# Kernel tuning notes

Hardware: AMD Instinct MI355X
Metric: run time of the kernel (lower is better)

## Reference

```python
import jax, jax.numpy as jnp
import numpy as np
import math

C = 512
H = W = 64
B = 4
NUM_GROUPS = 32
EPS = 1e-6
NUM_HEADS = 1  # num_head_channels=None -> 1 head


def group_norm(x, scale, bias):
    # x: [B, H, W, C] -> normalize per group of channels over (H, W, group-chans)
    b, h, w, c = x.shape
    xg = x.reshape(b, h, w, NUM_GROUPS, c // NUM_GROUPS)
    mean = xg.mean(axis=(1, 2, 4), keepdims=True)
    var = xg.var(axis=(1, 2, 4), keepdims=True)
    xg = (xg - mean) * jax.lax.rsqrt(var + EPS)
    x = xg.reshape(b, h, w, c)
    return x * scale + bias


def setup_inputs() -> dict:
    key = jax.random.key(0)
    ks = jax.random.split(key, 5)
    s = 1.0 / math.sqrt(C)
    return {
        "hidden_states": jax.random.normal(ks[0], (B, H, W, C), jnp.float32),
        "gn_scale": jnp.ones((C,), jnp.float32),
        "gn_bias": jnp.zeros((C,), jnp.float32),
        "Wq": jax.random.normal(ks[1], (C, C), jnp.float32) * s,
        "bq": jnp.zeros((C,), jnp.float32),
        "Wk": jax.random.normal(ks[2], (C, C), jnp.float32) * s,
        "bk": jnp.zeros((C,), jnp.float32),
        "Wv": jax.random.normal(ks[3], (C, C), jnp.float32) * s,
        "bv": jnp.zeros((C,), jnp.float32),
        "Wp": jax.random.normal(ks[4], (C, C), jnp.float32) * s,
        "bp": jnp.zeros((C,), jnp.float32),
    }


def reference(hidden_states, gn_scale, gn_bias, Wq, bq, Wk, bk, Wv, bv, Wp, bp):
    residual = hidden_states
    b, h, w, c = hidden_states.shape
    x = group_norm(hidden_states, gn_scale, gn_bias)
    x = x.reshape(b, h * w, c)  # [B, N, C]

    hd = c // NUM_HEADS
    def heads(t):  # [B, N, C] -> [B, nh, N, hd]
        return t.reshape(b, h * w, NUM_HEADS, hd).transpose(0, 2, 1, 3)

    q = heads(x @ Wq + bq)
    k = heads(x @ Wk + bk)
    v = heads(x @ Wv + bv)

    scale = 1.0 / math.sqrt(math.sqrt(c / NUM_HEADS))
    attn = jnp.einsum('bhqc,bhkc->bhqk', q * scale, k * scale)
    attn = jax.nn.softmax(attn, axis=-1)
    out = jnp.einsum('bhkc,bhqk->bhqc', v, attn)  # [B, nh, N, hd]
    out = out.transpose(0, 2, 1, 3).reshape(b, h * w, c)
    out = out @ Wp + bp
    out = out.reshape(b, h, w, c)
    return out + residual
```

## Files before the change

### kernel.cpp

```cpp
#include <hip/hip_runtime.h>
#include <hip/hip_bf16.h>

typedef __attribute__((ext_vector_type(8))) short bf16x8;
typedef __attribute__((ext_vector_type(4))) float f32x4;
typedef __attribute__((ext_vector_type(4))) unsigned short u16x4;

#define MFMA16(a, b, c) __builtin_amdgcn_mfma_f32_16x16x32_bf16(a, b, c, 0, 0, 0)

#define SCALE 0.21022410381342865f

__device__ __forceinline__ unsigned short f2bf(float f) {
    union { float f; unsigned u; } v; v.f = f;
    unsigned r = v.u + 0x7FFF + ((v.u >> 16) & 1);
    return (unsigned short)(r >> 16);
}

__device__ __forceinline__ unsigned cvtpk(float lo, float hi) {
    unsigned r;
    asm("v_cvt_pk_bf16_f32 %0, %1, %2" : "=v"(r) : "v"(lo), "v"(hi));
    return r;
}

typedef __attribute__((address_space(3))) void lds_void;
typedef const __attribute__((address_space(1))) void gbl_void;
__device__ __forceinline__ void g2l16(const void* g, void* l) {
    __builtin_amdgcn_global_load_lds((gbl_void*)g, (lds_void*)l, 16, 0, 0);
}

#define PHASE_BARRIER() do { \
    asm volatile("s_waitcnt vmcnt(0) lgkmcnt(0)" ::: "memory"); \
    __builtin_amdgcn_s_barrier(); \
    __builtin_amdgcn_sched_barrier(0); \
} while (0)

#define LGKM_BARRIER() do { \
    asm volatile("s_waitcnt lgkmcnt(0)" ::: "memory"); \
    __builtin_amdgcn_s_barrier(); \
    __builtin_amdgcn_sched_barrier(0); \
} while (0)

__global__ __launch_bounds__(256) void gn_stats(
    const float* __restrict__ x, float2* __restrict__ gstats)
{
    int id = blockIdx.x;
    int b = id >> 8, rem = id & 255;
    int g = rem >> 3, sl = rem & 7;
    int t = threadIdx.x;
    const float4* xf4 = (const float4*)x;
    size_t base4 = (size_t)b * (4096 * 128) + g * 4;

    float s = 0.f, ss = 0.f;
#pragma unroll
    for (int i = 0; i < 8; ++i) {
        int flat = i * 256 + t;
        int hw = sl * 512 + (flat >> 2), c4 = flat & 3;
        float4 v = xf4[base4 + (size_t)hw * 128 + c4];
        s  += v.x + v.y + v.z + v.w;
        ss += v.x * v.x + v.y * v.y + v.z * v.z + v.w * v.w;
    }
    for (int m = 32; m >= 1; m >>= 1) { s += __shfl_xor(s, m); ss += __shfl_xor(ss, m); }
    __shared__ float rs_[4], rss_[4];
    int wv = t >> 6;
    if ((t & 63) == 0) { rs_[wv] = s; rss_[wv] = ss; }
    __syncthreads();
    if (t == 0) {
        float2 o;
        o.x = rs_[0] + rs_[1] + rs_[2] + rs_[3];
        o.y = rss_[0] + rss_[1] + rss_[2] + rss_[3];
        gstats[id] = o;
    }
}

__global__ __launch_bounds__(256) void gn_apply(
    const float* __restrict__ x, const float* __restrict__ gamma,
    const float* __restrict__ beta, const float2* __restrict__ gstats,
    unsigned short* __restrict__ xn)
{
    int id = blockIdx.x;
    int b = id >> 9, rem = id & 511;
    int g = rem >> 4, sl = rem & 15;
    int t = threadIdx.x;

    float s = 0.f, ss = 0.f;
#pragma unroll
    for (int i = 0; i < 8; ++i) {
        float2 p = gstats[(b * 32 + g) * 8 + i];
        s += p.x; ss += p.y;
    }
    float mean = s * (1.f / 65536.f);
    float var  = ss * (1.f / 65536.f) - mean * mean;
    float rstd = rsqrtf(var + 1e-6f);

    const float4* xf4 = (const float4*)x;
    const float4* g4 = (const float4*)gamma;
    const float4* b4 = (const float4*)beta;
    size_t base4 = (size_t)b * (4096 * 128) + g * 4;
#pragma unroll
    for (int i = 0; i < 4; ++i) {
        int flat = i * 256 + t;
        int hw = sl * 256 + (flat >> 2), c4 = flat & 3;
        float4 v  = xf4[base4 + (size_t)hw * 128 + c4];
        float4 gm = g4[g * 4 + c4], bt = b4[g * 4 + c4];
        u16x4 o;
        o.x = f2bf((v.x - mean) * rstd * gm.x + bt.x);
        o.y = f2bf((v.y - mean) * rstd * gm.y + bt.y);
        o.z = f2bf((v.z - mean) * rstd * gm.z + bt.z);
        o.w = f2bf((v.w - mean) * rstd * gm.w + bt.w);
        *(u16x4*)&xn[(size_t)(b * 4096 + hw) * 512 + g * 16 + c4 * 4] = o;
    }
}

__global__ __launch_bounds__(256) void wprep(
    const float* __restrict__ Wq, const float* __restrict__ Wk,
    const float* __restrict__ Wv, const float* __restrict__ Wp,
    unsigned short* __restrict__ wqkvt, unsigned short* __restrict__ wpt)
{
    int idx = blockIdx.x * 256 + threadIdx.x;
    if (idx < 786432) {
        int n = idx >> 9, k = idx & 511;
        int j = n >> 9, nn = n & 511;
        const float* W = (j == 0) ? Wq : (j == 1) ? Wk : Wv;
        wqkvt[idx] = f2bf(W[k * 512 + nn]);
    } else {
        int i2 = idx - 786432;
        int n = i2 >> 9, k = i2 & 511;
        wpt[i2] = f2bf(Wp[k * 512 + n]);
    }
}

template <int MODE>
__global__ __launch_bounds__(256, 3) void gemm_kernel(
    const unsigned short* __restrict__ A, const unsigned short* __restrict__ Bt,
    const float* __restrict__ bias_q, const float* __restrict__ bias_k,
    const float* __restrict__ bias_v, const float* __restrict__ bias_p,
    const float* __restrict__ resid,
    unsigned short* __restrict__ Cbf, float* __restrict__ Cf)
{
    int m0 = blockIdx.x * 128;
    int n0 = blockIdx.y * 128;
    int t = threadIdx.x;
    int l = t & 63, w = t >> 6;
    int wm = w >> 1, wn = w & 1;
    int lr = l & 15, lg = l >> 4;

    __shared__ __align__(16) unsigned short lds[16384];
    unsigned short* As = lds;
    unsigned short* Bs = lds + 8192;

    const unsigned short* A_ = A + (size_t)m0 * 512;
    const unsigned short* B_ = Bt + (size_t)n0 * 512;

    auto stage = [&](int s) {
        int k0 = s * 64;
#pragma unroll
        for (int c = 0; c < 4; ++c) {
            int flat = c * 256 + t;
            int row = flat >> 3, u = flat & 7;
            g2l16(A_ + (size_t)row * 512 + k0 + ((u ^ (row & 7)) << 3),
                  As + (flat << 3));
        }
#pragma unroll
        for (int c = 0; c < 4; ++c) {
            int flat = c * 256 + t;
            int row = flat >> 3, u = flat & 7;
            g2l16(B_ + (size_t)row * 512 + k0 + ((u ^ (row & 7)) << 3),
                  Bs + (flat << 3));
        }
    };

    f32x4 acc[4][4];
#pragma unroll
    for (int i = 0; i < 4; ++i)
#pragma unroll
        for (int j = 0; j < 4; ++j) acc[i][j] = f32x4{0.f, 0.f, 0.f, 0.f};

    for (int s = 0; s < 8; ++s) {
        if (s) LGKM_BARRIER();
        stage(s);
        PHASE_BARRIER();
        __builtin_amdgcn_s_setprio(1);
#pragma unroll
        for (int ks = 0; ks < 2; ++ks) {
            bf16x8 af[4], bfr[4];
#pragma unroll
            for (int mi = 0; mi < 4; ++mi) {
                int row = wm * 64 + mi * 16 + lr;
                af[mi] = *(const bf16x8*)&As[(row * 8 + ((ks * 4 + lg) ^ (row & 7))) << 3];
            }
#pragma unroll
            for (int ni = 0; ni < 4; ++ni) {
                int row = wn * 64 + ni * 16 + lr;
                bfr[ni] = *(const bf16x8*)&Bs[(row * 8 + ((ks * 4 + lg) ^ (row & 7))) << 3];
            }
#pragma unroll
            for (int mi = 0; mi < 4; ++mi)
#pragma unroll
                for (int ni = 0; ni < 4; ++ni)
                    acc[mi][ni] = MFMA16(af[mi], bfr[ni], acc[mi][ni]);
        }
        __builtin_amdgcn_s_setprio(0);
    }

#pragma unroll
    for (int mi = 0; mi < 4; ++mi)
#pragma unroll
        for (int ni = 0; ni < 4; ++ni)
#pragma unroll
            for (int r = 0; r < 4; ++r) {
                int row = m0 + wm * 64 + mi * 16 + lg * 4 + r;
                int col = n0 + wn * 64 + ni * 16 + lr;
                float val = acc[mi][ni][r];
                if (MODE == 0) {
                    float bias, scl;
                    if (col < 512)       { bias = bias_q[col];        scl = SCALE; }
                    else if (col < 1024) { bias = bias_k[col - 512];  scl = SCALE; }
                    else                 { bias = bias_v[col - 1024]; scl = 1.0f;  }
                    Cbf[(size_t)row * 1536 + col] = f2bf((val + bias) * scl);
                } else {
                    Cf[(size_t)row * 512 + col] =
                        val + bias_p[col] + resid[(size_t)row * 512 + col];
                }
            }
}

__global__ __launch_bounds__(256) void vtrans(
    const unsigned short* __restrict__ qkv, unsigned short* __restrict__ vT)
{
    int n0 = blockIdx.x * 64, d0 = blockIdx.y * 64, b = blockIdx.z;
    int t = threadIdx.x;
    __shared__ unsigned short tile[64][72];
    for (int c = 0; c < 2; ++c) {
        int flat = c * 256 + t;
        int r = flat >> 3, cc = (flat & 7) * 8;
        *(bf16x8*)&tile[r][cc] =
            *(const bf16x8*)&qkv[(size_t)(b * 4096 + n0 + r) * 1536 + 1024 + d0 + cc];
    }
    __syncthreads();
    for (int c = 0; c < 2; ++c) {
        int flat = c * 256 + t;
        int dr = flat >> 3, nc = (flat & 7) * 8;
        bf16x8 v;
        for (int j = 0; j < 8; ++j) v[j] = (short)tile[nc + j][dr];
        *(bf16x8*)&vT[((size_t)b * 512 + d0 + dr) * 4096 + n0 + nc] = v;
    }
}

__global__ __launch_bounds__(256, 3) void qk_kernel(
    const unsigned short* __restrict__ qkv, unsigned short* __restrict__ P,
    float* __restrict__ lpart, int b0)
{
    int W = blockIdx.x;
    int xcd = W & 7, i = W >> 3;
    int bb = xcd >> 2;
    int nb = (xcd & 3) * 8 + (i & 7);
    int mb = i >> 3;
    int m0 = mb * 128, n0 = nb * 128;
    int b = b0 + bb;

    int t = threadIdx.x, l = t & 63, w = t >> 6;
    int wm = w >> 1, wn = w & 1;
    int lr = l & 15, lg = l >> 4;

    __shared__ __align__(16) unsigned short lds[16896];
    unsigned short* As = lds;
    unsigned short* Bs = lds + 8192;
    float* Lw = (float*)(lds + 16384);

    const unsigned short* A_ = qkv + (size_t)(b * 4096 + m0) * 1536 + 512;
    const unsigned short* B_ = qkv + (size_t)(b * 4096 + n0) * 1536;

    auto stage = [&](int s) {
        int k0 = s * 64;
#pragma unroll
        for (int c = 0; c < 4; ++c) {
            int flat = c * 256 + t;
            int row = flat >> 3, u = flat & 7;
            g2l16(A_ + (size_t)row * 1536 + k0 + ((u ^ (row & 7)) << 3),
                  As + (flat << 3));
        }
#pragma unroll
        for (int c = 0; c < 4; ++c) {
            int flat = c * 256 + t;
            int row = flat >> 3, u = flat & 7;
            g2l16(B_ + (size_t)row * 1536 + k0 + ((u ^ (row & 7)) << 3),
                  Bs + (flat << 3));
        }
    };

    f32x4 acc[4][4];
#pragma unroll
    for (int mi = 0; mi < 4; ++mi)
#pragma unroll
        for (int ni = 0; ni < 4; ++ni) acc[mi][ni] = f32x4{0.f, 0.f, 0.f, 0.f};

    for (int s = 0; s < 8; ++s) {
        if (s) LGKM_BARRIER();
        stage(s);
        PHASE_BARRIER();
        __builtin_amdgcn_s_setprio(1);
#pragma unroll
        for (int ks = 0; ks < 2; ++ks) {
            bf16x8 af[4], bfr[4];
#pragma unroll
            for (int mi = 0; mi < 4; ++mi) {
                int row = wm * 64 + mi * 16 + lr;
                af[mi] = *(const bf16x8*)&As[(row * 8 + ((ks * 4 + lg) ^ (row & 7))) << 3];
            }
#pragma unroll
            for (int ni = 0; ni < 4; ++ni) {
                int row = wn * 64 + ni * 16 + lr;
                bfr[ni] = *(const bf16x8*)&Bs[(row * 8 + ((ks * 4 + lg) ^ (row & 7))) << 3];
            }
#pragma unroll
            for (int mi = 0; mi < 4; ++mi)
#pragma unroll
                for (int ni = 0; ni < 4; ++ni)
                    acc[mi][ni] = MFMA16(af[mi], bfr[ni], acc[mi][ni]);
        }
        __builtin_amdgcn_s_setprio(0);
    }
    LGKM_BARRIER();

    unsigned short* Pl = lds;
    {
        float sums[4] = {0.f, 0.f, 0.f, 0.f};
#pragma unroll
        for (int mi = 0; mi < 4; ++mi) {
            int u = wm * 8 + mi * 2 + (lg >> 1);
            int half = lg & 1;
#pragma unroll
            for (int ni = 0; ni < 4; ++ni) {
                float p0 = __expf(acc[mi][ni][0]);
                float p1 = __expf(acc[mi][ni][1]);
                float p2 = __expf(acc[mi][ni][2]);
                float p3 = __expf(acc[mi][ni][3]);
                sums[ni] += p0 + p1 + p2 + p3;
                int q = wn * 64 + ni * 16 + lr;
                unsigned* dst = (unsigned*)&((char*)Pl)[
                    q * 256 + ((u ^ (q & 7)) << 4) + (half << 3)];
                dst[0] = cvtpk(p0, p1);
                dst[1] = cvtpk(p2, p3);
            }
        }
#pragma unroll
        for (int ni = 0; ni < 4; ++ni) {
            float v = sums[ni];
            v += __shfl_xor(v, 16);
            v += __shfl_xor(v, 32);
            if (lg == 0) Lw[wm * 128 + wn * 64 + ni * 16 + lr] = v;
        }
    }
    LGKM_BARRIER();

    if (t < 128)
        lpart[(size_t)(bb * 32 + mb) * 4096 + n0 + t] = Lw[t] + Lw[128 + t];

#pragma unroll
    for (int c = 0; c < 8; ++c) {
        int flat = c * 256 + t;
        int row = flat >> 4, u = flat & 15;
        *(bf16x8*)&P[((size_t)(bb * 4096 + n0 + row)) * 4096 + m0 + u * 8] =
            *(const bf16x8*)&((char*)Pl)[row * 256 + ((u ^ (row & 7)) << 4)];
    }
}

__global__ __launch_bounds__(256) void lred_kernel(
    const float* __restrict__ lpart, float* __restrict__ lsum)
{
    int rr = blockIdx.x * 256 + threadIdx.x;
    int bb = rr >> 12, r = rr & 4095;
    float s = 0.f;
#pragma unroll
    for (int sl = 0; sl < 32; ++sl)
        s += lpart[(size_t)(bb * 32 + sl) * 4096 + r];
    lsum[rr] = 1.0f / s;
}

__global__ __launch_bounds__(512) void pv_kernel(
    const unsigned short* __restrict__ P, const unsigned short* __restrict__ vT,
    const float* __restrict__ linv, unsigned short* __restrict__ outb, int b0)
{
    int m0 = blockIdx.x * 128, n0 = blockIdx.y * 128, bb = blockIdx.z;
    int b = b0 + bb;
    int t = threadIdx.x, l = t & 63, w = t >> 6;
    int wm = w >> 2, wn = w & 3;
    int lr = l & 15, lg = l >> 4;

    __shared__ __align__(16) unsigned short lds[49152];
    unsigned short* As = lds;
    unsigned short* Bs = lds + 24576;

    const unsigned short* A_ = P + (size_t)(bb * 4096 + m0) * 4096;
    const unsigned short* B_ = vT + ((size_t)b * 512 + n0) * 4096;

    auto stage = [&](int s, int buf) {
        int k0 = s * 64;
        unsigned short* ad = As + buf * 8192;
        unsigned short* bd = Bs + buf * 8192;
#pragma unroll
        for (int c = 0; c < 2; ++c) {
            int flat = c * 512 + t;
            int row = flat >> 3, u = flat & 7;
            g2l16(A_ + (size_t)row * 4096 + k0 + ((u ^ (row & 7)) << 3),
                  ad + (flat << 3));
        }
#pragma unroll
        for (int c = 0; c < 2; ++c) {
            int flat = c * 512 + t;
            int row = flat >> 3, u = flat & 7;
            g2l16(B_ + (size_t)row * 4096 + k0 + ((u ^ (row & 7)) << 3),
                  bd + (flat << 3));
        }
    };

    f32x4 acc[4][2];
#pragma unroll
    for (int i = 0; i < 4; ++i)
#pragma unroll
        for (int j = 0; j < 2; ++j) acc[i][j] = f32x4{0.f, 0.f, 0.f, 0.f};

    stage(0, 0);
    stage(1, 1);
    asm volatile("s_waitcnt vmcnt(4)" ::: "memory");
    __builtin_amdgcn_s_barrier();
    __builtin_amdgcn_sched_barrier(0);

    for (int s = 0; s < 64; ++s) {
        if (s + 2 < 64) stage(s + 2, (s + 2) % 3);
        const unsigned short* Al = As + (s % 3) * 8192;
        const unsigned short* Bl = Bs + (s % 3) * 8192;
        __builtin_amdgcn_s_setprio(1);
#pragma unroll
        for (int ks = 0; ks < 2; ++ks) {
            bf16x8 af[4], bfr[2];
#pragma unroll
            for (int mi = 0; mi < 4; ++mi) {
                int row = wm * 64 + mi * 16 + lr;
                af[mi] = *(const bf16x8*)&Al[(row * 8 + ((ks * 4 + lg) ^ (row & 7))) << 3];
            }
#pragma unroll
            for (int ni = 0; ni < 2; ++ni) {
                int row = wn * 32 + ni * 16 + lr;
                bfr[ni] = *(const bf16x8*)&Bl[(row * 8 + ((ks * 4 + lg) ^ (row & 7))) << 3];
            }
#pragma unroll
            for (int mi = 0; mi < 4; ++mi)
#pragma unroll
                for (int ni = 0; ni < 2; ++ni)
                    acc[mi][ni] = MFMA16(af[mi], bfr[ni], acc[mi][ni]);
        }
        __builtin_amdgcn_s_setprio(0);
        if (s < 62) asm volatile("s_waitcnt vmcnt(4) lgkmcnt(0)" ::: "memory");
        else        asm volatile("s_waitcnt vmcnt(0) lgkmcnt(0)" ::: "memory");
        __builtin_amdgcn_s_barrier();
        __builtin_amdgcn_sched_barrier(0);
    }

#pragma unroll
    for (int mi = 0; mi < 4; ++mi)
#pragma unroll
        for (int r = 0; r < 4; ++r) {
            int row = m0 + wm * 64 + mi * 16 + lg * 4 + r;
            float inv = linv[bb * 4096 + row];
#pragma unroll
            for (int ni = 0; ni < 2; ++ni) {
                int col = n0 + wn * 32 + ni * 16 + lr;
                outb[(size_t)(b * 4096 + row) * 512 + col] =
                    f2bf(acc[mi][ni][r] * inv);
            }
        }
}

extern "C" void kernel_launch(void* const* d_in, const int* in_sizes, int n_in,
                              void* d_out, int out_size, void* d_ws, size_t ws_size,
                              hipStream_t stream)
{
    const float* x     = (const float*)d_in[0];
    const float* gamma = (const float*)d_in[1];
    const float* beta  = (const float*)d_in[2];
    const float* Wq = (const float*)d_in[3];
    const float* bq = (const float*)d_in[4];
    const float* Wk = (const float*)d_in[5];
    const float* bk = (const float*)d_in[6];
    const float* Wv = (const float*)d_in[7];
    const float* bv = (const float*)d_in[8];
    const float* Wp = (const float*)d_in[9];
    const float* bp = (const float*)d_in[10];
    float* out = (float*)d_out;

    unsigned short* xn    = (unsigned short*)d_ws;
    unsigned short* wqkvt = xn + (size_t)16384 * 512;
    unsigned short* wpt   = wqkvt + (size_t)1536 * 512;
    unsigned short* qkv   = wpt + (size_t)512 * 512;
    unsigned short* vT    = qkv + (size_t)16384 * 1536;
    unsigned short* P     = vT + (size_t)4 * 512 * 4096;
    float* lpart = (float*)(P + (size_t)2 * 4096 * 4096);
    float* linv  = lpart + (size_t)128 * 4096;
    float2* gstats = (float2*)(linv + 8192);

    gn_stats<<<dim3(1024), dim3(256), 0, stream>>>(x, gstats);
    gn_apply<<<dim3(2048), dim3(256), 0, stream>>>(x, gamma, beta, gstats, xn);
    wprep<<<dim3(4096), dim3(256), 0, stream>>>(Wq, Wk, Wv, Wp, wqkvt, wpt);
    gemm_kernel<0><<<dim3(128, 12), dim3(256), 0, stream>>>(
        xn, wqkvt, bq, bk, bv, nullptr, nullptr, qkv, nullptr);
    vtrans<<<dim3(64, 8, 4), dim3(256), 0, stream>>>(qkv, vT);

    for (int b0 = 0; b0 < 4; b0 += 2) {
        qk_kernel<<<dim3(2048), dim3(256), 0, stream>>>(qkv, P, lpart, b0);
        lred_kernel<<<dim3(32), dim3(256), 0, stream>>>(lpart, linv);
        pv_kernel<<<dim3(32, 4, 2), dim3(512), 0, stream>>>(P, vT, linv, xn, b0);
    }

    gemm_kernel<1><<<dim3(128, 4), dim3(256), 0, stream>>>(
        xn, wpt, nullptr, nullptr, nullptr, bp, x, nullptr, out);
}
```

Before: 252.8 us.

## Enlarge QK tiles to 256x256 with double-buffered, phase-interleaved async loads

The QK^T kernel moves from 128x128 tiles with 256 threads to 256x256 tiles with 512 threads (8 waves), so the grid shrinks from 2048 to 512 blocks. Global-to-LDS loads are double-buffered and issued per half-tile, interleaved across four compute phases, with explicit vmcnt waits replacing the per-stage load-then-compute barrier. The larger tile raises operand reuse per byte loaded and hides load latency. In exchange it uses about 130KB of LDS (one block per CU), more accumulator registers and fewer blocks. The lpart partial-sum count and the reduction kernel are adjusted to match.

```diff
diff --git a/kernel.cpp b/kernel.cpp
--- a/kernel.cpp
+++ b/kernel.cpp
@@ -245,122 +245,165 @@
     }
 }
 
-__global__ __launch_bounds__(256, 3) void qk_kernel(
+__global__ __launch_bounds__(512, 1) void qk_kernel(
     const unsigned short* __restrict__ qkv, unsigned short* __restrict__ P,
     float* __restrict__ lpart, int b0)
 {
     int W = blockIdx.x;
     int xcd = W & 7, i = W >> 3;
     int bb = xcd >> 2;
-    int nb = (xcd & 3) * 8 + (i & 7);
-    int mb = i >> 3;
-    int m0 = mb * 128, n0 = nb * 128;
+    int nb = (xcd & 3) * 4 + (i & 3);
+    int mb = i >> 2;
+    int m0 = mb * 256, n0 = nb * 256;
     int b = b0 + bb;
 
     int t = threadIdx.x, l = t & 63, w = t >> 6;
-    int wm = w >> 1, wn = w & 1;
+    int wm = w >> 2, wn = w & 3;
     int lr = l & 15, lg = l >> 4;
 
-    __shared__ __align__(16) unsigned short lds[16896];
-    unsigned short* As = lds;
-    unsigned short* Bs = lds + 8192;
-    float* Lw = (float*)(lds + 16384);
-
-    const unsigned short* A_ = qkv + (size_t)(b * 4096 + m0) * 1536 + 512;
-    const unsigned short* B_ = qkv + (size_t)(b * 4096 + n0) * 1536;
-
-    auto stage = [&](int s) {
+    __shared__ __align__(16) unsigned short lds[66560];
+    float* Lw = (float*)(lds + 65536);
+
+    const unsigned short* Ksrc = qkv + 512;
+    const unsigned short* Qsrc = qkv;
+
+    auto stageA = [&](int s, int h) {
         int k0 = s * 64;
-#pragma unroll
-        for (int c = 0; c < 4; ++c) {
-            int flat = c * 256 + t;
+        unsigned short* dst = lds + ((s & 1) * 2 + h) * 8192;
+#pragma unroll
+        for (int c = 0; c < 2; ++c) {
+            int flat = c * 512 + t;
             int row = flat >> 3, u = flat & 7;
-            g2l16(A_ + (size_t)row * 1536 + k0 + ((u ^ (row & 7)) << 3),
-                  As + (flat << 3));
-        }
-#pragma unroll
-        for (int c = 0; c < 4; ++c) {
-            int flat = c * 256 + t;
+            int kv = m0 + h * 128 + row;
+            g2l16(Ksrc + (size_t)(b * 4096 + kv) * 1536 + k0 + ((u ^ (row & 7)) << 3),
+                  dst + (flat << 3));
+        }
+    };
+    auto stageB = [&](int s, int h) {
+        int k0 = s * 64;
+        unsigned short* dst = lds + 32768 + ((s & 1) * 2 + h) * 8192;
+#pragma unroll
+        for (int c = 0; c < 2; ++c) {
+            int flat = c * 512 + t;
             int row = flat >> 3, u = flat & 7;
-            g2l16(B_ + (size_t)row * 1536 + k0 + ((u ^ (row & 7)) << 3),
-                  Bs + (flat << 3));
+            int q = n0 + h * 128 + row;
+            g2l16(Qsrc + (size_t)(b * 4096 + q) * 1536 + k0 + ((u ^ (row & 7)) << 3),
+                  dst + (flat << 3));
         }
     };
 
-    f32x4 acc[4][4];
-#pragma unroll
-    for (int mi = 0; mi < 4; ++mi)
+    f32x4 acc[8][4];
+#pragma unroll
+    for (int mi = 0; mi < 8; ++mi)
 #pragma unroll
         for (int ni = 0; ni < 4; ++ni) acc[mi][ni] = f32x4{0.f, 0.f, 0.f, 0.f};
 
+    stageA(0, 0); stageA(0, 1); stageB(0, 0); stageB(0, 1);
+    stageA(1, 0); stageB(1, 0);
+    asm volatile("s_waitcnt vmcnt(4)" ::: "memory");
+    __builtin_amdgcn_s_barrier();
+    __builtin_amdgcn_sched_barrier(0);
+
     for (int s = 0; s < 8; ++s) {
-        if (s) LGKM_BARRIER();
-        stage(s);
-        PHASE_BARRIER();
-        __builtin_amdgcn_s_setprio(1);
-#pragma unroll
-        for (int ks = 0; ks < 2; ++ks) {
-            bf16x8 af[4], bfr[4];
+#pragma unroll
+        for (int ph = 0; ph < 4; ++ph) {
+            const int mh = ph & 1, nh = ph >> 1;
+            const unsigned short* Abase = lds + ((s & 1) * 2 + mh) * 8192;
+            const unsigned short* Bbase = lds + 32768 + ((s & 1) * 2 + nh) * 8192;
+            bf16x8 af[4][2], bfr[2][2];
 #pragma unroll
             for (int mi = 0; mi < 4; ++mi) {
                 int row = wm * 64 + mi * 16 + lr;
-                af[mi] = *(const bf16x8*)&As[(row * 8 + ((ks * 4 + lg) ^ (row & 7))) << 3];
-            }
-#pragma unroll
-            for (int ni = 0; ni < 4; ++ni) {
-                int row = wn * 64 + ni * 16 + lr;
-                bfr[ni] = *(const bf16x8*)&Bs[(row * 8 + ((ks * 4 + lg) ^ (row & 7))) << 3];
-            }
+#pragma unroll
+                for (int ks = 0; ks < 2; ++ks)
+                    af[mi][ks] = *(const bf16x8*)&Abase[
+                        (row * 8 + ((ks * 4 + lg) ^ (row & 7))) << 3];
+            }
+#pragma unroll
+            for (int ni = 0; ni < 2; ++ni) {
+                int row = wn * 32 + ni * 16 + lr;
+#pragma unroll
+                for (int ks = 0; ks < 2; ++ks)
+                    bfr[ni][ks] = *(const bf16x8*)&Bbase[
+                        (row * 8 + ((ks * 4 + lg) ^ (row & 7))) << 3];
+            }
+            if (ph == 0) { if (s + 1 < 8) stageA(s + 1, 1); }
+            if (ph == 1) { if (s + 1 < 8) stageB(s + 1, 1); }
+            if (ph == 2) { if (s + 2 < 8) stageB(s + 2, 0); }
+            if (ph == 3) { if (s + 2 < 8) stageA(s + 2, 0); }
+
+            __builtin_amdgcn_s_barrier();
+            asm volatile("s_waitcnt lgkmcnt(0)" ::: "memory");
+            __builtin_amdgcn_sched_barrier(0);
+
+            __builtin_amdgcn_s_setprio(1);
 #pragma unroll
             for (int mi = 0; mi < 4; ++mi)
 #pragma unroll
-                for (int ni = 0; ni < 4; ++ni)
-                    acc[mi][ni] = MFMA16(af[mi], bfr[ni], acc[mi][ni]);
-        }
-        __builtin_amdgcn_s_setprio(0);
-    }
-    LGKM_BARRIER();
+                for (int ni = 0; ni < 2; ++ni)
+#pragma unroll
+                    for (int ks = 0; ks < 2; ++ks)
+                        acc[mh * 4 + mi][nh * 2 + ni] =
+                            MFMA16(af[mi][ks], bfr[ni][ks], acc[mh * 4 + mi][nh * 2 + ni]);
+            __builtin_amdgcn_s_setprio(0);
+
+            if (s < 6 || (s == 6 && ph < 2))
+                asm volatile("s_waitcnt vmcnt(8)" ::: "memory");
+            else
+                asm volatile("s_waitcnt vmcnt(0)" ::: "memory");
+            __builtin_amdgcn_s_barrier();
+            __builtin_amdgcn_sched_barrier(0);
+        }
+    }
 
     unsigned short* Pl = lds;
     {
         float sums[4] = {0.f, 0.f, 0.f, 0.f};
 #pragma unroll
-        for (int mi = 0; mi < 4; ++mi) {
-            int u = wm * 8 + mi * 2 + (lg >> 1);
-            int half = lg & 1;
-#pragma unroll
-            for (int ni = 0; ni < 4; ++ni) {
-                float p0 = __expf(acc[mi][ni][0]);
-                float p1 = __expf(acc[mi][ni][1]);
-                float p2 = __expf(acc[mi][ni][2]);
-                float p3 = __expf(acc[mi][ni][3]);
-                sums[ni] += p0 + p1 + p2 + p3;
-                int q = wn * 64 + ni * 16 + lr;
-                unsigned* dst = (unsigned*)&((char*)Pl)[
-                    q * 256 + ((u ^ (q & 7)) << 4) + (half << 3)];
-                dst[0] = cvtpk(p0, p1);
-                dst[1] = cvtpk(p2, p3);
-            }
-        }
-#pragma unroll
-        for (int ni = 0; ni < 4; ++ni) {
-            float v = sums[ni];
-            v += __shfl_xor(v, 16);
-            v += __shfl_xor(v, 32);
-            if (lg == 0) Lw[wm * 128 + wn * 64 + ni * 16 + lr] = v;
-        }
+        for (int mh = 0; mh < 2; ++mh)
+#pragma unroll
+            for (int mi = 0; mi < 4; ++mi) {
+                int u = mh * 16 + wm * 8 + mi * 2 + (lg >> 1);
+                int half = lg & 1;
+#pragma unroll
+                for (int nh = 0; nh < 2; ++nh)
+#pragma unroll
+                    for (int ni = 0; ni < 2; ++ni) {
+                        int j = nh * 2 + ni;
+                        float p0 = __expf(acc[mh * 4 + mi][j][0]);
+                        float p1 = __expf(acc[mh * 4 + mi][j][1]);
+                        float p2 = __expf(acc[mh * 4 + mi][j][2]);
+                        float p3 = __expf(acc[mh * 4 + mi][j][3]);
+                        sums[j] += p0 + p1 + p2 + p3;
+                        int qL = nh * 128 + wn * 32 + ni * 16 + lr;
+                        unsigned* dst = (unsigned*)&((char*)Pl)[
+                            qL * 512 + ((u ^ (qL & 7)) << 4) + (half << 3)];
+                        dst[0] = cvtpk(p0, p1);
+                        dst[1] = cvtpk(p2, p3);
+                    }
+            }
+#pragma unroll
+        for (int nh = 0; nh < 2; ++nh)
+#pragma unroll
+            for (int ni = 0; ni < 2; ++ni) {
+                float v = sums[nh * 2 + ni];
+                v += __shfl_xor(v, 16);
+                v += __shfl_xor(v, 32);
+                if (lg == 0)
+                    Lw[wm * 256 + nh * 128 + wn * 32 + ni * 16 + lr] = v;
+            }
     }
     LGKM_BARRIER();
 
-    if (t < 128)
-        lpart[(size_t)(bb * 32 + mb) * 4096 + n0 + t] = Lw[t] + Lw[128 + t];
-
-#pragma unroll
-    for (int c = 0; c < 8; ++c) {
-        int flat = c * 256 + t;
-        int row = flat >> 4, u = flat & 15;
+    if (t < 256)
+        lpart[(size_t)(bb * 16 + mb) * 4096 + n0 + t] = Lw[t] + Lw[256 + t];
+
+#pragma unroll
+    for (int c = 0; c < 16; ++c) {
+        int flat = c * 512 + t;
+        int row = flat >> 5, u = flat & 31;
         *(bf16x8*)&P[((size_t)(bb * 4096 + n0 + row)) * 4096 + m0 + u * 8] =
-            *(const bf16x8*)&((char*)Pl)[row * 256 + ((u ^ (row & 7)) << 4)];
+            *(const bf16x8*)&((char*)Pl)[row * 512 + ((u ^ (row & 7)) << 4)];
     }
 }
 
@@ -371,8 +414,8 @@
     int bb = rr >> 12, r = rr & 4095;
     float s = 0.f;
 #pragma unroll
-    for (int sl = 0; sl < 32; ++sl)
-        s += lpart[(size_t)(bb * 32 + sl) * 4096 + r];
+    for (int sl = 0; sl < 16; ++sl)
+        s += lpart[(size_t)(bb * 16 + sl) * 4096 + r];
     lsum[rr] = 1.0f / s;
 }
 
@@ -506,7 +549,7 @@
     vtrans<<<dim3(64, 8, 4), dim3(256), 0, stream>>>(qkv, vT);
 
     for (int b0 = 0; b0 < 4; b0 += 2) {
-        qk_kernel<<<dim3(2048), dim3(256), 0, stream>>>(qkv, P, lpart, b0);
+        qk_kernel<<<dim3(512), dim3(512), 0, stream>>>(qkv, P, lpart, b0);
         lred_kernel<<<dim3(32), dim3(256), 0, stream>>>(lpart, linv);
         pv_kernel<<<dim3(32, 4, 2), dim3(512), 0, stream>>>(P, vT, linv, xn, b0);
     }
```

After: 265.3 us. +4.9%, slower.
